# Performance work log

Hardware: AMD Instinct MI355X
Metric: run time of the kernel (lower is better)

The kernel has to match this reference:

```python
import jax, jax.numpy as jnp
import numpy as np

N = 100000      # num nodes
R = 32          # num relations
E = 3200000     # num edges
F_IN = 128      # feat_len
H = 16          # hidden dim (hard-coded in source)
C = 8           # num classes


def setup_inputs() -> dict:
    key = jax.random.key(0)
    k1, k2, k3, k4, k5 = jax.random.split(key, 5)
    emb = jax.random.normal(k1, (N, F_IN), dtype=jnp.float32)
    W1 = jax.random.normal(k2, (R, F_IN, H), dtype=jnp.float32) * 0.05
    W2 = jax.random.normal(k3, (R, H, C), dtype=jnp.float32) * 0.05
    edge_index = jax.random.randint(k4, (2, E), 0, N, dtype=jnp.int64)
    edge_type = jax.random.randint(k5, (E,), 0, R, dtype=jnp.int64)
    return {"emb": emb, "W1": W1, "W2": W2,
            "edge_index": edge_index, "edge_type": edge_type}


def _rgcn_layer(x, W, src, dst, etype, edge_norm):
    # x: [N, Fin], W: [R, Fin, Fout]
    # Transform once per relation, then gather per edge (avoids [E,Fin,Fout]).
    xw = jnp.einsum('nf,rfo->rno', x, W)          # [R, N, Fout]
    msg = xw[etype, src] * edge_norm[:, None]      # [E, Fout]
    return jax.ops.segment_sum(msg, dst, num_segments=N)  # [N, Fout]


def reference(emb, W1, W2, edge_index, edge_type):
    src, dst = edge_index[0], edge_index[1]
    # PyG RGCNConv aggr='mean': normalize by per-(dst, relation) in-degree.
    key_idx = dst * R + edge_type                              # [E]
    deg = jax.ops.segment_sum(jnp.ones((E,), emb.dtype), key_idx,
                              num_segments=N * R)              # [N*R]
    edge_norm = 1.0 / jnp.maximum(deg, 1.0)
    edge_norm = edge_norm[key_idx]                             # [E]

    h = jax.nn.relu(_rgcn_layer(emb, W1, src, dst, edge_type, edge_norm))
    h = _rgcn_layer(h, W2, src, dst, edge_type, edge_norm)
    return jax.nn.log_softmax(h, axis=1)
```

## Files before the change

### kernel.cpp

```cpp
#include <hip/hip_runtime.h>
#include <hip/hip_bf16.h>
#include <math.h>

#define N_NODES 100000
#define R 32
#define E_EDGES 3200000
#define F_IN 128
#define HDIM 16
#define CDIM 8
#define NOUT 512
#define M_PAD 100032
#define NBUCK 391
#define CAP 9216
#define KEYS 8192
#define P1CHUNK 8192
#define CVT_BLKS 6252
#define PREP_BLKS 128
#define FRONT_GRID (NBUCK + CVT_BLKS + PREP_BLKS)
#define GEMM_BLKS 1563
#define MID_GRID (NBUCK + GEMM_BLKS)

typedef __attribute__((ext_vector_type(8))) short bf16x8;
typedef __attribute__((ext_vector_type(4))) float f32x4;
typedef __attribute__((ext_vector_type(2))) _Float16 f16x2;

static __device__ __forceinline__ unsigned short f2bf(float f) {
    unsigned int u = __float_as_uint(f);
    unsigned int r = (u + 0x7FFFu + ((u >> 16) & 1u)) >> 16;
    return (unsigned short)r;
}
static __device__ __forceinline__ float bfl(unsigned x) {
    return __uint_as_float(x << 16);
}
static __device__ __forceinline__ float bfh(unsigned x) {
    return __uint_as_float(x & 0xFFFF0000u);
}
static __device__ __forceinline__ f16x2 asf16x2(float f) {
    union { float f; f16x2 h; } u; u.f = f; return u.h;
}

#if __has_builtin(__builtin_amdgcn_fdot2)
static __device__ __forceinline__ float FDOT2(f16x2 a, f16x2 b, float c) {
    return __builtin_amdgcn_fdot2(a, b, c, false);
}
#else
static __device__ __forceinline__ float FDOT2(f16x2 a, f16x2 b, float c) {
    return c + (float)a.x * (float)b.x + (float)a.y * (float)b.y;
}
#endif

__global__ __launch_bounds__(512) void k_front(const int* __restrict__ src,
                                               const int* __restrict__ dst,
                                               const int* __restrict__ et,
                                               const float* __restrict__ emb,
                                               const float* __restrict__ W1,
                                               int* __restrict__ gcursor,
                                               unsigned int* __restrict__ ebuf,
                                               unsigned short* __restrict__ ebf,
                                               unsigned short* __restrict__ BmT) {
    __shared__ int sh[3 * NBUCK];
    int b = blockIdx.x, t = threadIdx.x;
    if (b < NBUCK) {
        int* hist = sh;
        int* rank = sh + NBUCK;
        int* base = sh + 2 * NBUCK;
        for (int j = t; j < NBUCK; j += 512) { hist[j] = 0; rank[j] = 0; }
        __syncthreads();
        int e0 = b * P1CHUNK;
        int e1 = e0 + P1CHUNK; if (e1 > E_EDGES) e1 = E_EDGES;
        int n4 = (e1 - e0) >> 2;
        const int4* d4 = (const int4*)(dst + e0);
        const int4* s4 = (const int4*)(src + e0);
        const int4* t4 = (const int4*)(et + e0);
        for (int i = t; i < n4; i += 512) {
            int4 v = d4[i];
            atomicAdd(&hist[v.x >> 8], 1);
            atomicAdd(&hist[v.y >> 8], 1);
            atomicAdd(&hist[v.z >> 8], 1);
            atomicAdd(&hist[v.w >> 8], 1);
        }
        __syncthreads();
        for (int j = t; j < NBUCK; j += 512)
            base[j] = hist[j] ? atomicAdd(&gcursor[j], hist[j]) : 0;
        __syncthreads();
        for (int i = t; i < n4; i += 512) {
            int4 dv = d4[i];
            int4 sv = s4[i];
            int4 tv = t4[i];
            int ds[4] = {dv.x, dv.y, dv.z, dv.w};
            int ss[4] = {sv.x, sv.y, sv.z, sv.w};
            int ts[4] = {tv.x, tv.y, tv.z, tv.w};
            #pragma unroll
            for (int u = 0; u < 4; ++u) {
                int d = ds[u];
                int bk = d >> 8;
                unsigned pk = ((unsigned)(d & 255) << 22) | ((unsigned)ts[u] << 17)
                            | (unsigned)ss[u];
                int lr = atomicAdd(&rank[bk], 1);
                ebuf[(size_t)bk * CAP + base[bk] + lr] = pk;
            }
        }
    } else if (b < NBUCK + CVT_BLKS) {
        size_t base = ((size_t)(b - NBUCK) * 512 + t) * 4;
        int row = (int)(base >> 7);
        ushort4 o;
        if (row < N_NODES) {
            float4 a = *(const float4*)(emb + base);
            o.x = f2bf(a.x); o.y = f2bf(a.y); o.z = f2bf(a.z); o.w = f2bf(a.w);
        } else {
            o.x = o.y = o.z = o.w = 0;
        }
        *(ushort4*)(ebf + base) = o;
    } else {
        int i = (b - NBUCK - CVT_BLKS) * 512 + t;
        int n = i >> 7;
        int f = i & 127;
        int r = n >> 4;
        int o = n & 15;
        BmT[i] = f2bf(W1[r * (F_IN * HDIM) + f * HDIM + o]);
    }
}

__global__ __launch_bounds__(512) void k_scanb(const int* __restrict__ gcursor,
                                               int* __restrict__ bucketstart,
                                               int* __restrict__ rowstart) {
    __shared__ int sb[NBUCK + 1];
    int t = threadIdx.x;
    if (t == 0) {
        int acc = 0;
        for (int b = 0; b < NBUCK; ++b) { int v = gcursor[b]; sb[b] = acc; acc += v; }
        sb[NBUCK] = acc;
        rowstart[N_NODES] = acc;
    }
    __syncthreads();
    for (int j = t; j <= NBUCK; j += 512) bucketstart[j] = sb[j];
}

__global__ __launch_bounds__(256) void k_mid(const unsigned int* __restrict__ ebuf,
                                             const int* __restrict__ gcursor,
                                             const int* __restrict__ bucketstart,
                                             int* __restrict__ rowstart,
                                             unsigned int* __restrict__ elist,
                                             const unsigned short* __restrict__ Abf,
                                             const unsigned short* __restrict__ BmT,
                                             unsigned short* __restrict__ C) {
    __shared__ __align__(16) char smem[52224 + 64];
    int b = blockIdx.x, t = threadIdx.x;
    if (b < NBUCK) {
        unsigned int* cnt = (unsigned int*)smem;
        int* wsum = (int*)(smem + 32768);
        int cntE = gcursor[b];
        size_t esrc = (size_t)b * CAP;
        int e0 = bucketstart[b];
        #pragma unroll
        for (int j = 0; j < KEYS / 256; ++j) cnt[t + j * 256] = 0;
        __syncthreads();
        for (int i = t; i < cntE; i += 256)
            atomicAdd(&cnt[ebuf[esrc + i] >> 17], 1u);
        __syncthreads();
        int kbase = t * (KEYS / 256);
        int s = 0;
        #pragma unroll
        for (int j = 0; j < KEYS / 256; ++j) s += (int)cnt[kbase + j];
        int lane = t & 63, wv = t >> 6;
        int sc = s;
        #pragma unroll
        for (int off = 1; off < 64; off <<= 1) {
            int v = __shfl_up(sc, off, 64);
            if (lane >= off) sc += v;
        }
        if (lane == 63) wsum[wv] = sc;
        __syncthreads();
        if (t == 0) {
            int a = 0;
            #pragma unroll
            for (int w = 0; w < 4; ++w) { int v = wsum[w]; wsum[w] = a; a += v; }
        }
        __syncthreads();
        int run = wsum[wv] + sc - s;
        #pragma unroll
        for (int j = 0; j < KEYS / 256; ++j) {
            unsigned v = cnt[kbase + j];
            unsigned lc = v > 1023u ? 1023u : v;
            cnt[kbase + j] = (unsigned)run | (lc << 20);
            run += (int)v;
        }
        __syncthreads();
        {
            int d = b * 256 + t;
            if (d < N_NODES) rowstart[d] = e0 + (int)(cnt[t * 32] & 0xFFFFFu);
        }
        __syncthreads();
        for (int i = t; i < cntE; i += 256) {
            unsigned pk = ebuf[esrc + i];
            int key = pk >> 17;
            unsigned vv = atomicAdd(&cnt[key], 1u);
            int pos = (int)(vv & 0xFFFFFu);
            unsigned len = (vv >> 20) & 1023u;
            elist[e0 + pos] = (pk & 0x3FFFFFu) | (len << 22);
        }
    } else {
        unsigned short* As = (unsigned short*)smem;
        unsigned short* Bs = (unsigned short*)(smem + 17408);
        int row0 = (b - NBUCK) * 64;
        #pragma unroll
        for (int j = 0; j < 4; ++j) {
            int idx = t + j * 256;
            int r = idx >> 4;
            int u = idx & 15;
            float4 v = *(const float4*)(Abf + (size_t)(row0 + r) * F_IN + u * 8);
            *(float4*)(&As[r * 136 + u * 8]) = v;
        }
        int w = t >> 6;
        int lane = t & 63;
        int q = lane >> 4;
        int mr = lane & 15;
        const unsigned short* ap = &As[(w * 16 + mr) * 136 + q * 8];
        for (int col0 = 0; col0 < NOUT; col0 += 128) {
            __syncthreads();
            #pragma unroll
            for (int j = 0; j < 8; ++j) {
                int idx = t + j * 256;
                int r = idx >> 4;
                int u = idx & 15;
                float4 v = *(const float4*)(BmT + (size_t)(col0 + r) * F_IN + u * 8);
                *(float4*)(&Bs[r * 136 + u * 8]) = v;
            }
            __syncthreads();
            f32x4 acc[8] = {};
            #pragma unroll
            for (int kk = 0; kk < 4; ++kk) {
                bf16x8 af = *(const bf16x8*)(ap + kk * 32);
                #pragma unroll
                for (int tt = 0; tt < 8; ++tt) {
                    bf16x8 bf = *(const bf16x8*)(&Bs[(tt * 16 + mr) * 136 + q * 8 + kk * 32]);
                    acc[tt] = __builtin_amdgcn_mfma_f32_16x16x32_bf16(af, bf, acc[tt], 0, 0, 0);
                }
            }
            #pragma unroll
            for (int tt = 0; tt < 8; ++tt) {
                #pragma unroll
                for (int j = 0; j < 4; ++j) {
                    int row = row0 + w * 16 + q * 4 + j;
                    C[(size_t)row * NOUT + col0 + tt * 16 + mr] = f2bf(acc[tt][j]);
                }
            }
        }
    }
}

__global__ __launch_bounds__(256) void k_gather1(const int* __restrict__ rowstart,
                                                 const unsigned int* __restrict__ elist,
                                                 const unsigned short* __restrict__ xw1,
                                                 _Float16* __restrict__ h) {
    __shared__ float nlut[1024];
    int t = threadIdx.x;
    for (int j = t; j < 1024; j += 256) nlut[j] = 1.0f / (float)(j ? j : 1);
    __syncthreads();
    int g = t >> 3;
    int c = t & 7;
    int d = blockIdx.x * 32 + g;
    if (d >= N_NODES) return;
    int i = rowstart[d], end = rowstart[d + 1];
    float a0 = 0.f, a1 = 0.f, b0 = 0.f, b1 = 0.f;
    float c0 = 0.f, c1 = 0.f, e0 = 0.f, e1 = 0.f;
    for (; i + 3 < end; i += 4) {
        unsigned pk0 = elist[i];
        unsigned pk1 = elist[i + 1];
        unsigned pk2 = elist[i + 2];
        unsigned pk3 = elist[i + 3];
        unsigned x0 = *(const unsigned*)(xw1 + (size_t)(pk0 & 0x1FFFF) * NOUT + ((pk0 >> 17) & 31) * HDIM + c * 2);
        unsigned x1 = *(const unsigned*)(xw1 + (size_t)(pk1 & 0x1FFFF) * NOUT + ((pk1 >> 17) & 31) * HDIM + c * 2);
        unsigned x2 = *(const unsigned*)(xw1 + (size_t)(pk2 & 0x1FFFF) * NOUT + ((pk2 >> 17) & 31) * HDIM + c * 2);
        unsigned x3 = *(const unsigned*)(xw1 + (size_t)(pk3 & 0x1FFFF) * NOUT + ((pk3 >> 17) & 31) * HDIM + c * 2);
        float n0 = nlut[pk0 >> 22], n1 = nlut[pk1 >> 22];
        float n2 = nlut[pk2 >> 22], n3 = nlut[pk3 >> 22];
        a0 += bfl(x0) * n0; a1 += bfh(x0) * n0;
        b0 += bfl(x1) * n1; b1 += bfh(x1) * n1;
        c0 += bfl(x2) * n2; c1 += bfh(x2) * n2;
        e0 += bfl(x3) * n3; e1 += bfh(x3) * n3;
    }
    for (; i < end; ++i) {
        unsigned pk = elist[i];
        unsigned x = *(const unsigned*)(xw1 + (size_t)(pk & 0x1FFFF) * NOUT + ((pk >> 17) & 31) * HDIM + c * 2);
        float nm = nlut[pk >> 22];
        a0 += bfl(x) * nm; a1 += bfh(x) * nm;
    }
    f16x2 o;
    o.x = (_Float16)fmaxf(a0 + b0 + c0 + e0, 0.f);
    o.y = (_Float16)fmaxf(a1 + b1 + c1 + e1, 0.f);
    *(f16x2*)(h + (size_t)d * HDIM + c * 2) = o;
}

#define W2P 260
__global__ __launch_bounds__(256) void k_gather2(const int* __restrict__ rowstart,
                                                 const unsigned int* __restrict__ elist,
                                                 const _Float16* __restrict__ h,
                                                 const float* __restrict__ W2,
                                                 float* __restrict__ out) {
    __shared__ f16x2 sW2h[CDIM * W2P];
    __shared__ float nlut[1024];
    int t = threadIdx.x;
    for (int j = t; j < 1024; j += 256) nlut[j] = 1.0f / (float)(j ? j : 1);
    #pragma unroll
    for (int j = 0; j < 8; ++j) {
        int idx = t + j * 256;
        int c = idx >> 8;
        int rem = idx & 255;
        int r = rem >> 3;
        int jj = rem & 7;
        f16x2 p;
        p.x = (_Float16)W2[r * (HDIM * CDIM) + (2 * jj) * CDIM + c];
        p.y = (_Float16)W2[r * (HDIM * CDIM) + (2 * jj + 1) * CDIM + c];
        sW2h[c * W2P + rem] = p;
    }
    __syncthreads();

    int g = t >> 3;
    int c = t & 7;
    int d = blockIdx.x * 32 + g;
    if (d >= N_NODES) return;
    const f16x2* wc = &sW2h[c * W2P];
    int i = rowstart[d], end = rowstart[d + 1];
    float acc0 = 0.f, acc1 = 0.f, acc2 = 0.f, acc3 = 0.f;
    for (; i + 3 < end; i += 4) {
        unsigned pk0 = elist[i];
        unsigned pk1 = elist[i + 1];
        unsigned pk2 = elist[i + 2];
        unsigned pk3 = elist[i + 3];
        const float4* hp0 = (const float4*)(h + (size_t)(pk0 & 0x1FFFF) * HDIM);
        const float4* hp1 = (const float4*)(h + (size_t)(pk1 & 0x1FFFF) * HDIM);
        const float4* hp2 = (const float4*)(h + (size_t)(pk2 & 0x1FFFF) * HDIM);
        const float4* hp3 = (const float4*)(h + (size_t)(pk3 & 0x1FFFF) * HDIM);
        float4 u0 = hp0[0], u1 = hp0[1];
        float4 v0 = hp1[0], v1 = hp1[1];
        float4 w0 = hp2[0], w1 = hp2[1];
        float4 x0 = hp3[0], x1 = hp3[1];
        float nm0 = nlut[pk0 >> 22], nm1 = nlut[pk1 >> 22];
        float nm2 = nlut[pk2 >> 22], nm3 = nlut[pk3 >> 22];
        const f16x2* wp0 = wc + ((pk0 >> 17) & 31) * 8;
        const f16x2* wp1 = wc + ((pk1 >> 17) & 31) * 8;
        const f16x2* wp2 = wc + ((pk2 >> 17) & 31) * 8;
        const f16x2* wp3 = wc + ((pk3 >> 17) & 31) * 8;
        float s0 = 0.f, s1 = 0.f, s2 = 0.f, s3 = 0.f;
        s0 = FDOT2(asf16x2(u0.x), wp0[0], s0);
        s0 = FDOT2(asf16x2(u0.y), wp0[1], s0);
        s0 = FDOT2(asf16x2(u0.z), wp0[2], s0);
        s0 = FDOT2(asf16x2(u0.w), wp0[3], s0);
        s0 = FDOT2(asf16x2(u1.x), wp0[4], s0);
        s0 = FDOT2(asf16x2(u1.y), wp0[5], s0);
        s0 = FDOT2(asf16x2(u1.z), wp0[6], s0);
        s0 = FDOT2(asf16x2(u1.w), wp0[7], s0);
        s1 = FDOT2(asf16x2(v0.x), wp1[0], s1);
        s1 = FDOT2(asf16x2(v0.y), wp1[1], s1);
        s1 = FDOT2(asf16x2(v0.z), wp1[2], s1);
        s1 = FDOT2(asf16x2(v0.w), wp1[3], s1);
        s1 = FDOT2(asf16x2(v1.x), wp1[4], s1);
        s1 = FDOT2(asf16x2(v1.y), wp1[5], s1);
        s1 = FDOT2(asf16x2(v1.z), wp1[6], s1);
        s1 = FDOT2(asf16x2(v1.w), wp1[7], s1);
        s2 = FDOT2(asf16x2(w0.x), wp2[0], s2);
        s2 = FDOT2(asf16x2(w0.y), wp2[1], s2);
        s2 = FDOT2(asf16x2(w0.z), wp2[2], s2);
        s2 = FDOT2(asf16x2(w0.w), wp2[3], s2);
        s2 = FDOT2(asf16x2(w1.x), wp2[4], s2);
        s2 = FDOT2(asf16x2(w1.y), wp2[5], s2);
        s2 = FDOT2(asf16x2(w1.z), wp2[6], s2);
        s2 = FDOT2(asf16x2(w1.w), wp2[7], s2);
        s3 = FDOT2(asf16x2(x0.x), wp3[0], s3);
        s3 = FDOT2(asf16x2(x0.y), wp3[1], s3);
        s3 = FDOT2(asf16x2(x0.z), wp3[2], s3);
        s3 = FDOT2(asf16x2(x0.w), wp3[3], s3);
        s3 = FDOT2(asf16x2(x1.x), wp3[4], s3);
        s3 = FDOT2(asf16x2(x1.y), wp3[5], s3);
        s3 = FDOT2(asf16x2(x1.z), wp3[6], s3);
        s3 = FDOT2(asf16x2(x1.w), wp3[7], s3);
        acc0 += nm0 * s0;
        acc1 += nm1 * s1;
        acc2 += nm2 * s2;
        acc3 += nm3 * s3;
    }
    for (; i < end; ++i) {
        unsigned pk = elist[i];
        const float4* hp = (const float4*)(h + (size_t)(pk & 0x1FFFF) * HDIM);
        float4 u0 = hp[0], u1 = hp[1];
        float nm = nlut[pk >> 22];
        const f16x2* wp = wc + ((pk >> 17) & 31) * 8;
        float sd = 0.f;
        sd = FDOT2(asf16x2(u0.x), wp[0], sd);
        sd = FDOT2(asf16x2(u0.y), wp[1], sd);
        sd = FDOT2(asf16x2(u0.z), wp[2], sd);
        sd = FDOT2(asf16x2(u0.w), wp[3], sd);
        sd = FDOT2(asf16x2(u1.x), wp[4], sd);
        sd = FDOT2(asf16x2(u1.y), wp[5], sd);
        sd = FDOT2(asf16x2(u1.z), wp[6], sd);
        sd = FDOT2(asf16x2(u1.w), wp[7], sd);
        acc0 += nm * sd;
    }
    float acc = (acc0 + acc1) + (acc2 + acc3);
    float m = acc;
    #pragma unroll
    for (int mask = 1; mask < 8; mask <<= 1)
        m = fmaxf(m, __shfl_xor(m, mask, 8));
    float ex = expf(acc - m);
    float ssumv = ex;
    #pragma unroll
    for (int mask = 1; mask < 8; mask <<= 1)
        ssumv += __shfl_xor(ssumv, mask, 8);
    out[(size_t)d * CDIM + c] = acc - m - logf(ssumv);
}

extern "C" void kernel_launch(void* const* d_in, const int* in_sizes, int n_in,
                              void* d_out, int out_size, void* d_ws, size_t ws_size,
                              hipStream_t stream) {
    const float* emb = (const float*)d_in[0];
    const float* W1  = (const float*)d_in[1];
    const float* W2  = (const float*)d_in[2];
    const int* ei    = (const int*)d_in[3];
    const int* et    = (const int*)d_in[4];
    const int* srcp  = ei;
    const int* dstp  = ei + E_EDGES;

    char* ws = (char*)d_ws;
    size_t off = 0;
    #define ALIGN256(x) (((x) + 255) & ~(size_t)255)
    int* gcursor     = (int*)(ws + off); off = ALIGN256(off + 512 * 4);
    int* bucketstart = (int*)(ws + off); off = ALIGN256(off + 512 * 4);
    int* rowstart    = (int*)(ws + off); off = ALIGN256(off + ((size_t)N_NODES + 8) * 4);
    unsigned int* ebuf  = (unsigned int*)(ws + off); off = ALIGN256(off + (size_t)NBUCK * CAP * 4);
    unsigned int* elist = (unsigned int*)(ws + off); off = ALIGN256(off + (size_t)E_EDGES * 4);
    unsigned short* BmT  = (unsigned short*)(ws + off); off = ALIGN256(off + (size_t)NOUT * F_IN * 2);
    unsigned short* ebf  = (unsigned short*)(ws + off); off = ALIGN256(off + (size_t)M_PAD * F_IN * 2);
    unsigned short* xw1  = (unsigned short*)(ws + off); off = ALIGN256(off + (size_t)M_PAD * NOUT * 2);
    _Float16* h          = (_Float16*)(ws + off);       off = ALIGN256(off + (size_t)N_NODES * HDIM * 2);
    float* out = (float*)d_out;

    hipMemsetAsync(gcursor, 0, 512 * 4, stream);

    k_front<<<FRONT_GRID, 512, 0, stream>>>(srcp, dstp, et, emb, W1, gcursor, ebuf, ebf, BmT);
    k_scanb<<<1, 512, 0, stream>>>(gcursor, bucketstart, rowstart);
    k_mid<<<MID_GRID, 256, 0, stream>>>(ebuf, gcursor, bucketstart, rowstart, elist, ebf, BmT, xw1);
    k_gather1<<<(N_NODES + 31) / 32, 256, 0, stream>>>(rowstart, elist, xw1, h);
    k_gather2<<<(N_NODES + 31) / 32, 256, 0, stream>>>(rowstart, elist, h, W2, out);
}
```

Measured before the change: 328.3 us.

## Drop scan kernel and bf16 emb pass; fuse conversion into GEMM tile load

Removes the single-block bucket scan kernel by keeping the edge list in fixed-capacity per-bucket slots and storing explicit (start,end) row ranges. The emb-to-bf16 conversion pass is dropped, and the GEMM loads fp32 emb directly and converts to bf16 when staging into shared memory. The front kernel now uses smaller edge chunks with 256-thread blocks for more parallelism. This saves one launch, one serial scan and a full write/read of the bf16 embedding copy. The costs are a padded edge list with gaps between buckets and twice the global read bytes in the GEMM A load.

New measurement: 363.0 us. +10.6%, slower.

```diff
diff --git a/kernel.cpp b/kernel.cpp
--- a/kernel.cpp
+++ b/kernel.cpp
@@ -13,10 +13,10 @@
 #define NBUCK 391
 #define CAP 9216
 #define KEYS 8192
-#define P1CHUNK 8192
-#define CVT_BLKS 6252
-#define PREP_BLKS 128
-#define FRONT_GRID (NBUCK + CVT_BLKS + PREP_BLKS)
+#define P1CHUNK 2048
+#define NCHK ((E_EDGES + P1CHUNK - 1) / P1CHUNK)
+#define PREP_BLKS 256
+#define FRONT_GRID (NCHK + PREP_BLKS)
 #define GEMM_BLKS 1563
 #define MID_GRID (NBUCK + GEMM_BLKS)
 
@@ -49,22 +49,20 @@
 }
 #endif
 
-__global__ __launch_bounds__(512) void k_front(const int* __restrict__ src,
+__global__ __launch_bounds__(256) void k_front(const int* __restrict__ src,
                                                const int* __restrict__ dst,
                                                const int* __restrict__ et,
-                                               const float* __restrict__ emb,
                                                const float* __restrict__ W1,
                                                int* __restrict__ gcursor,
                                                unsigned int* __restrict__ ebuf,
-                                               unsigned short* __restrict__ ebf,
                                                unsigned short* __restrict__ BmT) {
     __shared__ int sh[3 * NBUCK];
     int b = blockIdx.x, t = threadIdx.x;
-    if (b < NBUCK) {
+    if (b < NCHK) {
         int* hist = sh;
         int* rank = sh + NBUCK;
         int* base = sh + 2 * NBUCK;
-        for (int j = t; j < NBUCK; j += 512) { hist[j] = 0; rank[j] = 0; }
+        for (int j = t; j < NBUCK; j += 256) { hist[j] = 0; rank[j] = 0; }
         __syncthreads();
         int e0 = b * P1CHUNK;
         int e1 = e0 + P1CHUNK; if (e1 > E_EDGES) e1 = E_EDGES;
@@ -72,7 +70,7 @@
         const int4* d4 = (const int4*)(dst + e0);
         const int4* s4 = (const int4*)(src + e0);
         const int4* t4 = (const int4*)(et + e0);
-        for (int i = t; i < n4; i += 512) {
+        for (int i = t; i < n4; i += 256) {
             int4 v = d4[i];
             atomicAdd(&hist[v.x >> 8], 1);
             atomicAdd(&hist[v.y >> 8], 1);
@@ -80,10 +78,10 @@
             atomicAdd(&hist[v.w >> 8], 1);
         }
         __syncthreads();
-        for (int j = t; j < NBUCK; j += 512)
+        for (int j = t; j < NBUCK; j += 256)
             base[j] = hist[j] ? atomicAdd(&gcursor[j], hist[j]) : 0;
         __syncthreads();
-        for (int i = t; i < n4; i += 512) {
+        for (int i = t; i < n4; i += 256) {
             int4 dv = d4[i];
             int4 sv = s4[i];
             int4 tv = t4[i];
@@ -100,19 +98,8 @@
                 ebuf[(size_t)bk * CAP + base[bk] + lr] = pk;
             }
         }
-    } else if (b < NBUCK + CVT_BLKS) {
-        size_t base = ((size_t)(b - NBUCK) * 512 + t) * 4;
-        int row = (int)(base >> 7);
-        ushort4 o;
-        if (row < N_NODES) {
-            float4 a = *(const float4*)(emb + base);
-            o.x = f2bf(a.x); o.y = f2bf(a.y); o.z = f2bf(a.z); o.w = f2bf(a.w);
-        } else {
-            o.x = o.y = o.z = o.w = 0;
-        }
-        *(ushort4*)(ebf + base) = o;
     } else {
-        int i = (b - NBUCK - CVT_BLKS) * 512 + t;
+        int i = (b - NCHK) * 256 + t;
         int n = i >> 7;
         int f = i & 127;
         int r = n >> 4;
@@ -121,27 +108,11 @@
     }
 }
 
-__global__ __launch_bounds__(512) void k_scanb(const int* __restrict__ gcursor,
-                                               int* __restrict__ bucketstart,
-                                               int* __restrict__ rowstart) {
-    __shared__ int sb[NBUCK + 1];
-    int t = threadIdx.x;
-    if (t == 0) {
-        int acc = 0;
-        for (int b = 0; b < NBUCK; ++b) { int v = gcursor[b]; sb[b] = acc; acc += v; }
-        sb[NBUCK] = acc;
-        rowstart[N_NODES] = acc;
-    }
-    __syncthreads();
-    for (int j = t; j <= NBUCK; j += 512) bucketstart[j] = sb[j];
-}
-
 __global__ __launch_bounds__(256) void k_mid(const unsigned int* __restrict__ ebuf,
                                              const int* __restrict__ gcursor,
-                                             const int* __restrict__ bucketstart,
-                                             int* __restrict__ rowstart,
+                                             int2* __restrict__ rse,
                                              unsigned int* __restrict__ elist,
-                                             const unsigned short* __restrict__ Abf,
+                                             const float* __restrict__ A,
                                              const unsigned short* __restrict__ BmT,
                                              unsigned short* __restrict__ C) {
     __shared__ __align__(16) char smem[52224 + 64];
@@ -150,13 +121,12 @@
         unsigned int* cnt = (unsigned int*)smem;
         int* wsum = (int*)(smem + 32768);
         int cntE = gcursor[b];
-        size_t esrc = (size_t)b * CAP;
-        int e0 = bucketstart[b];
+        size_t e0 = (size_t)b * CAP;
         #pragma unroll
         for (int j = 0; j < KEYS / 256; ++j) cnt[t + j * 256] = 0;
         __syncthreads();
         for (int i = t; i < cntE; i += 256)
-            atomicAdd(&cnt[ebuf[esrc + i] >> 17], 1u);
+            atomicAdd(&cnt[ebuf[e0 + i] >> 17], 1u);
         __syncthreads();
         int kbase = t * (KEYS / 256);
         int s = 0;
@@ -188,11 +158,15 @@
         __syncthreads();
         {
             int d = b * 256 + t;
-            if (d < N_NODES) rowstart[d] = e0 + (int)(cnt[t * 32] & 0xFFFFFu);
+            if (d < N_NODES) {
+                int rs = (int)(cnt[t * 32] & 0xFFFFFu);
+                int re = (t < 255) ? (int)(cnt[(t + 1) * 32] & 0xFFFFFu) : cntE;
+                rse[d] = make_int2((int)e0 + rs, (int)e0 + re);
+            }
         }
         __syncthreads();
         for (int i = t; i < cntE; i += 256) {
-            unsigned pk = ebuf[esrc + i];
+            unsigned pk = ebuf[e0 + i];
             int key = pk >> 17;
             unsigned vv = atomicAdd(&cnt[key], 1u);
             int pos = (int)(vv & 0xFFFFFu);
@@ -204,12 +178,16 @@
         unsigned short* Bs = (unsigned short*)(smem + 17408);
         int row0 = (b - NBUCK) * 64;
         #pragma unroll
-        for (int j = 0; j < 4; ++j) {
+        for (int j = 0; j < 8; ++j) {
             int idx = t + j * 256;
-            int r = idx >> 4;
-            int u = idx & 15;
-            float4 v = *(const float4*)(Abf + (size_t)(row0 + r) * F_IN + u * 8);
-            *(float4*)(&As[r * 136 + u * 8]) = v;
+            int r = idx >> 5;
+            int u = idx & 31;
+            int grow = row0 + r;
+            float4 v = make_float4(0.f, 0.f, 0.f, 0.f);
+            if (grow < N_NODES) v = *(const float4*)(A + (size_t)grow * F_IN + u * 4);
+            ushort4 o;
+            o.x = f2bf(v.x); o.y = f2bf(v.y); o.z = f2bf(v.z); o.w = f2bf(v.w);
+            *(ushort4*)(&As[r * 136 + u * 4]) = o;
         }
         int w = t >> 6;
         int lane = t & 63;
@@ -249,7 +227,7 @@
     }
 }
 
-__global__ __launch_bounds__(256) void k_gather1(const int* __restrict__ rowstart,
+__global__ __launch_bounds__(256) void k_gather1(const int2* __restrict__ rse,
                                                  const unsigned int* __restrict__ elist,
                                                  const unsigned short* __restrict__ xw1,
                                                  _Float16* __restrict__ h) {
@@ -261,7 +239,8 @@
     int c = t & 7;
     int d = blockIdx.x * 32 + g;
     if (d >= N_NODES) return;
-    int i = rowstart[d], end = rowstart[d + 1];
+    int2 rr = rse[d];
+    int i = rr.x, end = rr.y;
     float a0 = 0.f, a1 = 0.f, b0 = 0.f, b1 = 0.f;
     float c0 = 0.f, c1 = 0.f, e0 = 0.f, e1 = 0.f;
     for (; i + 3 < end; i += 4) {
@@ -293,7 +272,7 @@
 }
 
 #define W2P 260
-__global__ __launch_bounds__(256) void k_gather2(const int* __restrict__ rowstart,
+__global__ __launch_bounds__(256) void k_gather2(const int2* __restrict__ rse,
                                                  const unsigned int* __restrict__ elist,
                                                  const _Float16* __restrict__ h,
                                                  const float* __restrict__ W2,
@@ -321,7 +300,8 @@
     int d = blockIdx.x * 32 + g;
     if (d >= N_NODES) return;
     const f16x2* wc = &sW2h[c * W2P];
-    int i = rowstart[d], end = rowstart[d + 1];
+    int2 rr = rse[d];
+    int i = rr.x, end = rr.y;
     float acc0 = 0.f, acc1 = 0.f, acc2 = 0.f, acc3 = 0.f;
     for (; i + 3 < end; i += 4) {
         unsigned pk0 = elist[i];
@@ -425,21 +405,18 @@
     size_t off = 0;
     #define ALIGN256(x) (((x) + 255) & ~(size_t)255)
     int* gcursor     = (int*)(ws + off); off = ALIGN256(off + 512 * 4);
-    int* bucketstart = (int*)(ws + off); off = ALIGN256(off + 512 * 4);
-    int* rowstart    = (int*)(ws + off); off = ALIGN256(off + ((size_t)N_NODES + 8) * 4);
+    int2* rse        = (int2*)(ws + off); off = ALIGN256(off + ((size_t)N_NODES + 8) * 8);
     unsigned int* ebuf  = (unsigned int*)(ws + off); off = ALIGN256(off + (size_t)NBUCK * CAP * 4);
-    unsigned int* elist = (unsigned int*)(ws + off); off = ALIGN256(off + (size_t)E_EDGES * 4);
+    unsigned int* elist = (unsigned int*)(ws + off); off = ALIGN256(off + (size_t)NBUCK * CAP * 4);
     unsigned short* BmT  = (unsigned short*)(ws + off); off = ALIGN256(off + (size_t)NOUT * F_IN * 2);
-    unsigned short* ebf  = (unsigned short*)(ws + off); off = ALIGN256(off + (size_t)M_PAD * F_IN * 2);
     unsigned short* xw1  = (unsigned short*)(ws + off); off = ALIGN256(off + (size_t)M_PAD * NOUT * 2);
     _Float16* h          = (_Float16*)(ws + off);       off = ALIGN256(off + (size_t)N_NODES * HDIM * 2);
     float* out = (float*)d_out;
 
     hipMemsetAsync(gcursor, 0, 512 * 4, stream);
 
-    k_front<<<FRONT_GRID, 512, 0, stream>>>(srcp, dstp, et, emb, W1, gcursor, ebuf, ebf, BmT);
-    k_scanb<<<1, 512, 0, stream>>>(gcursor, bucketstart, rowstart);
-    k_mid<<<MID_GRID, 256, 0, stream>>>(ebuf, gcursor, bucketstart, rowstart, elist, ebf, BmT, xw1);
-    k_gather1<<<(N_NODES + 31) / 32, 256, 0, stream>>>(rowstart, elist, xw1, h);
-    k_gather2<<<(N_NODES + 31) / 32, 256, 0, stream>>>(rowstart, elist, h, W2, out);
-}
+    k_front<<<FRONT_GRID, 256, 0, stream>>>(srcp, dstp, et, W1, gcursor, ebuf, BmT);
+    k_mid<<<MID_GRID, 256, 0, stream>>>(ebuf, gcursor, rse, elist, emb, BmT, xw1);
+    k_gather1<<<(N_NODES + 31) / 32, 256, 0, stream>>>(rse, elist, xw1, h);
+    k_gather2<<<(N_NODES + 31) / 32, 256, 0, stream>>>(rse, elist, h, W2, out);
+}
```
